# Kernel optimization log

Measured on AMD Instinct MI355X. Metric: run time of the kernel, lower is better.

## Reference

```python
import jax, jax.numpy as jnp
import numpy as np

N = 200000          # nodes
E = 6_400_000       # edges (avg degree 32)
F = 128             # num_node_features
H = 16              # GCN hidden width (hard-coded in module)
MLP_H = 100         # lin1 width (hard-coded)
C = 27              # num_classes (SIDER labels)
G = 4096            # number of graphs in the batch


def setup_inputs() -> dict:
    key = jax.random.key(0)
    ks = jax.random.split(key, 12)
    x = jax.random.normal(ks[0], (N, F), dtype=jnp.float32)
    edge_index = jax.random.randint(ks[1], (2, E), 0, N, dtype=jnp.int64)
    batch_vec = jnp.sort(jax.random.randint(ks[2], (N,), 0, G, dtype=jnp.int64))
    s = 0.05
    W1 = jax.random.normal(ks[3], (F, H), dtype=jnp.float32) * s
    b1 = jnp.zeros((H,), jnp.float32)
    W2 = jax.random.normal(ks[4], (H, H), dtype=jnp.float32) * s
    b2 = jnp.zeros((H,), jnp.float32)
    Wl1 = jax.random.normal(ks[5], (H, MLP_H), dtype=jnp.float32) * s
    bl1 = jnp.zeros((MLP_H,), jnp.float32)
    Wl2 = jax.random.normal(ks[6], (MLP_H, C), dtype=jnp.float32) * s
    bl2 = jnp.zeros((C,), jnp.float32)
    return dict(x=x, edge_index=edge_index, batch_vec=batch_vec,
                W1=W1, b1=b1, W2=W2, b2=b2, Wl1=Wl1, bl1=bl1, Wl2=Wl2, bl2=bl2)


def reference(x, edge_index, batch_vec, W1, b1, W2, b2, Wl1, bl1, Wl2, bl2):
    # PyG GCNConv: add self-loops, symmetric D^-1/2 (A+I) D^-1/2 normalization.
    src, dst = edge_index[0], edge_index[1]
    loop = jnp.arange(N, dtype=edge_index.dtype)
    src_f = jnp.concatenate([src, loop])   # [E+N]
    dst_f = jnp.concatenate([dst, loop])
    deg = jax.ops.segment_sum(jnp.ones(E + N, jnp.float32), dst_f, num_segments=N)
    dinv = jax.lax.rsqrt(deg)              # deg >= 1 due to self-loops
    norm = dinv[src_f] * dinv[dst_f]       # [E+N]

    def gcn_conv(h, W, b):
        h = h @ W                                       # transform first (cheaper: H=16)
        msg = h[src_f] * norm[:, None]                  # gather + scale  [E+N, H]
        return jax.ops.segment_sum(msg, dst_f, num_segments=N) + b

    h = jax.nn.relu(gcn_conv(x, W1, b1))   # dropout: identity in eval mode
    h = gcn_conv(h, W2, b2)
    g = jax.ops.segment_sum(h, batch_vec, num_segments=G)  # global_add_pool [G,H]
    g = jax.nn.relu(g)
    g = jax.nn.relu(g @ Wl1 + bl1)
    return g @ Wl2 + bl2                   # logits [G, C]
```

## Files before the change

### kernel.cpp

```cpp
#include <hip/hip_runtime.h>
#include <hip/hip_bf16.h>

#define NNODES 200000
#define NEDGES 6400000
#define NFEAT  128
#define NH     16
#define NMLP   100
#define NCLS   27
#define NGRAPH 4096

#define BKTSH  10
#define BKTW   1024
#define NBKT   ((NNODES + BKTW - 1) / BKTW)
#define NBLKA  256
#define ABLK   1024
#define EPB    (NEDGES / NBLKA)
#define HSZ    (NBKT * NBLKA)
#define SCANB  1024
#define NSCAN2 ((HSZ + SCANB - 1) / SCANB)
#define CAP    34816

__device__ __forceinline__ unsigned short f2bf(float f) {
    unsigned u = __float_as_uint(f);
    return (unsigned short)((u + 0x7FFF + ((u >> 16) & 1)) >> 16);
}
__device__ __forceinline__ float bf2f(unsigned short s) {
    return __uint_as_float(((unsigned)s) << 16);
}

__global__ __launch_bounds__(ABLK) void k_histA(const int* __restrict__ dst,
                                                int* __restrict__ H) {
    __shared__ int hist[NBKT];
    int tid = threadIdx.x, k = blockIdx.x;
    for (int b = tid; b < NBKT; b += ABLK) hist[b] = 0;
    __syncthreads();
    int base = k * EPB;
    #pragma unroll 4
    for (int i = tid; i < EPB; i += ABLK) {
        int d = __builtin_nontemporal_load(dst + base + i);
        atomicAdd(&hist[d >> BKTSH], 1);
    }
    __syncthreads();
    for (int b = tid; b < NBKT; b += ABLK) H[b * NBLKA + k] = hist[b];
}

__global__ __launch_bounds__(256) void k_scan_part(const int* __restrict__ A,
                                                   int* __restrict__ bsum) {
    __shared__ int sd[256];
    int tid = threadIdx.x;
    int i0 = blockIdx.x * SCANB + tid * 4;
    int s = 0;
    #pragma unroll
    for (int u = 0; u < 4; ++u) {
        int i = i0 + u;
        if (i < HSZ) s += A[i];
    }
    sd[tid] = s;
    __syncthreads();
    for (int off = 128; off > 0; off >>= 1) {
        if (tid < off) sd[tid] += sd[tid + off];
        __syncthreads();
    }
    if (tid == 0) bsum[blockIdx.x] = sd[0];
}

__global__ __launch_bounds__(256) void k_scan_top(int* __restrict__ bsum,
                                                  float* __restrict__ G,
                                                  int* __restrict__ cipad) {
    float4* G4 = (float4*)G;
    int tid = threadIdx.x;
    #pragma unroll
    for (int t = 0; t < (NGRAPH * NH / 4) / 256; ++t)
        G4[tid + t * 256] = make_float4(0.f, 0.f, 0.f, 0.f);
    if (tid < 64) cipad[tid] = 0;

    __shared__ int sd[256];
    int i0 = tid * 4;
    int c[4];
    #pragma unroll
    for (int u = 0; u < 4; ++u) {
        int i = i0 + u;
        c[u] = (i < NSCAN2) ? bsum[i] : 0;
    }
    int mysum = c[0] + c[1] + c[2] + c[3];
    sd[tid] = mysum;
    __syncthreads();
    for (int off = 1; off < 256; off <<= 1) {
        int v = (tid >= off) ? sd[tid - off] : 0;
        __syncthreads();
        sd[tid] += v;
        __syncthreads();
    }
    int base = sd[tid] - mysum;
    #pragma unroll
    for (int u = 0; u < 4; ++u) {
        int i = i0 + u;
        if (i < NSCAN2) { bsum[i] = base; base += c[u]; }
    }
}

__global__ __launch_bounds__(256) void k_scan_final(int* __restrict__ A,
                                                    const int* __restrict__ bsum) {
    __shared__ int sd[256];
    int tid = threadIdx.x;
    int i0 = blockIdx.x * SCANB + tid * 4;
    int c[4];
    #pragma unroll
    for (int u = 0; u < 4; ++u) {
        int i = i0 + u;
        c[u] = (i < HSZ) ? A[i] : 0;
    }
    int mysum = c[0] + c[1] + c[2] + c[3];
    sd[tid] = mysum;
    __syncthreads();
    for (int off = 1; off < 256; off <<= 1) {
        int v = (tid >= off) ? sd[tid - off] : 0;
        __syncthreads();
        sd[tid] += v;
        __syncthreads();
    }
    int base = bsum[blockIdx.x] + sd[tid] - mysum;
    #pragma unroll
    for (int u = 0; u < 4; ++u) {
        int i = i0 + u;
        if (i < HSZ) { A[i] = base; base += c[u]; }
    }
}

__global__ __launch_bounds__(ABLK) void k_scatterA(const int* __restrict__ src,
                                                   const int* __restrict__ dst,
                                                   const int* __restrict__ S,
                                                   int* __restrict__ P) {
    __shared__ int cnt[NBKT];
    int tid = threadIdx.x, k = blockIdx.x;
    for (int b = tid; b < NBKT; b += ABLK) cnt[b] = S[b * NBLKA + k];
    __syncthreads();
    int base = k * EPB;
    #pragma unroll 4
    for (int i = tid; i < EPB; i += ABLK) {
        int d = __builtin_nontemporal_load(dst + base + i);
        int s = __builtin_nontemporal_load(src + base + i);
        int pos = atomicAdd(&cnt[d >> BKTSH], 1);
        P[pos] = ((d & (BKTW - 1)) << 18) | s;
    }
}

__global__ __launch_bounds__(ABLK) void k_csrB(const int* __restrict__ P,
                                               const int* __restrict__ S,
                                               int* __restrict__ rp,
                                               float* __restrict__ dinv,
                                               int* __restrict__ colidx) {
    __shared__ int outl[CAP];
    __shared__ int deg[BKTW];
    __shared__ int wp[BKTW];
    __shared__ int sc[BKTW];
    __shared__ int se[2];
    int b = blockIdx.x, tid = threadIdx.x;
    if (tid == 0) {
        se[0] = S[b * NBLKA];
        se[1] = (b == NBKT - 1) ? NEDGES : S[(b + 1) * NBLKA];
    }
    deg[tid] = 0;
    __syncthreads();
    int start = se[0], end = se[1];

    for (int i = start + tid; i < end; i += ABLK)
        atomicAdd(&deg[P[i] >> 18], 1);
    __syncthreads();

    int myc = deg[tid];
    sc[tid] = myc;
    __syncthreads();
    for (int off = 1; off < BKTW; off <<= 1) {
        int v = (tid >= off) ? sc[tid - off] : 0;
        __syncthreads();
        sc[tid] += v;
        __syncthreads();
    }
    wp[tid] = start + sc[tid] - myc;
    int node = b * BKTW + tid;
    if (node < NNODES) {
        rp[node]   = wp[tid];
        dinv[node] = rsqrtf(1.f + (float)myc);
    }
    if (b == 0 && tid == 0) rp[NNODES] = NEDGES;
    __syncthreads();

    for (int i = start + tid; i < end; i += ABLK) {
        int v = P[i];
        int pos = atomicAdd(&wp[v >> 18], 1);
        int rel = pos - start;
        if (rel < CAP) outl[rel] = v & 0x3FFFF;
        else           colidx[pos] = v & 0x3FFFF;
    }
    __syncthreads();

    int cnt = end - start;
    if (cnt > CAP) cnt = CAP;
    for (int i = tid; i < cnt; i += ABLK)
        colidx[start + i] = outl[i];
}

#define GROWS 64
#define GPAD  129
__global__ __launch_bounds__(256) void k_gemm1(const float* __restrict__ x,
                                               const float* __restrict__ W1,
                                               const float* __restrict__ dinv,
                                               unsigned short* __restrict__ A1b) {
    __shared__ float xt[GROWS * GPAD];
    __shared__ float Ws[NFEAT * NH];
    int tid = threadIdx.x;
    int r0 = blockIdx.x * GROWS;

    #pragma unroll
    for (int t = 0; t < (NFEAT * NH) / 256; ++t)
        Ws[tid + t * 256] = W1[tid + t * 256];

    const float4* xg = (const float4*)(x + (size_t)r0 * NFEAT);
    #pragma unroll
    for (int t = 0; t < (GROWS * NFEAT / 4) / 256; ++t) {
        int fi = tid + t * 256;
        float4 v = xg[fi];
        int row = fi >> 5;
        int c4  = fi & 31;
        float* p = &xt[row * GPAD + c4 * 4];
        p[0] = v.x; p[1] = v.y; p[2] = v.z; p[3] = v.w;
    }
    __syncthreads();

    int r  = tid >> 2;
    int jq = tid & 3;
    float4 acc = make_float4(0.f, 0.f, 0.f, 0.f);
    #pragma unroll 8
    for (int k = 0; k < NFEAT; ++k) {
        float xv = xt[r * GPAD + k];
        float4 w = *(const float4*)&Ws[k * NH + jq * 4];
        acc.x += xv * w.x; acc.y += xv * w.y;
        acc.z += xv * w.z; acc.w += xv * w.w;
    }
    int n = r0 + r;
    float s = dinv[n];
    ushort4 o;
    o.x = f2bf(acc.x * s); o.y = f2bf(acc.y * s);
    o.z = f2bf(acc.z * s); o.w = f2bf(acc.w * s);
    *(ushort4*)&A1b[(size_t)n * NH + jq * 4] = o;
}

__global__ __launch_bounds__(256) void k_gather1(const unsigned short* __restrict__ A1b,
                                                 const int* __restrict__ rp,
                                                 const int* __restrict__ ci,
                                                 const float* __restrict__ dinv,
                                                 const float* __restrict__ b1,
                                                 const float* __restrict__ W2,
                                                 unsigned short* __restrict__ A2b) {
    __shared__ float W2s[NH * NH];
    __shared__ float b1s[NH];
    int tid = threadIdx.x;
    if (tid < NH * NH) W2s[tid] = W2[tid];
    if (tid < NH)      b1s[tid] = b1[tid];
    __syncthreads();

    int nl = tid >> 4, j = tid & 15;
    int n  = blockIdx.x * 16 + nl;
    int r0 = rp[n], r1 = rp[n + 1];

    float acc = bf2f(A1b[(size_t)n * NH + j]);
    for (int k = r0; k < r1; k += 16) {
        int   c[16];
        float v[16];
        #pragma unroll
        for (int u = 0; u < 16; ++u) c[u] = ci[k + u];
        #pragma unroll
        for (int u = 0; u < 16; ++u) v[u] = bf2f(A1b[(size_t)c[u] * NH + j]);
        #pragma unroll
        for (int u = 0; u < 16; ++u) acc += (k + u < r1) ? v[u] : 0.f;
    }

    float h = fmaxf(acc * dinv[n] + b1s[j], 0.f);
    float o = 0.f;
    #pragma unroll
    for (int kk = 0; kk < NH; ++kk)
        o += __shfl(h, kk, 16) * W2s[kk * NH + j];
    A2b[(size_t)n * NH + j] = f2bf(o * dinv[n]);
}

__global__ __launch_bounds__(256) void k_gather2(const unsigned short* __restrict__ A2b,
                                                 const int* __restrict__ rp,
                                                 const int* __restrict__ ci,
                                                 const float* __restrict__ dinv,
                                                 const float* __restrict__ b2,
                                                 const int* __restrict__ batch,
                                                 float* __restrict__ G) {
    __shared__ float b2s[NH];
    int tid = threadIdx.x;
    if (tid < NH) b2s[tid] = b2[tid];
    __syncthreads();

    int nl = tid >> 4, j = tid & 15;
    int n  = blockIdx.x * 16 + nl;
    int r0 = rp[n], r1 = rp[n + 1];

    float acc = bf2f(A2b[(size_t)n * NH + j]);
    for (int k = r0; k < r1; k += 16) {
        int   c[16];
        float v[16];
        #pragma unroll
        for (int u = 0; u < 16; ++u) c[u] = ci[k + u];
        #pragma unroll
        for (int u = 0; u < 16; ++u) v[u] = bf2f(A2b[(size_t)c[u] * NH + j]);
        #pragma unroll
        for (int u = 0; u < 16; ++u) acc += (k + u < r1) ? v[u] : 0.f;
    }

    float h2 = acc * dinv[n] + b2s[j];
    atomicAdd(&G[(size_t)batch[n] * NH + j], h2);
}

__global__ __launch_bounds__(128) void k_head(const float* __restrict__ G,
                                              const float* __restrict__ Wl1,
                                              const float* __restrict__ bl1,
                                              const float* __restrict__ Wl2,
                                              const float* __restrict__ bl2,
                                              float* __restrict__ out) {
    __shared__ float gv[NH];
    __shared__ float g1[NMLP];
    int g = blockIdx.x, tid = threadIdx.x;

    if (tid < NH) gv[tid] = fmaxf(G[(size_t)g * NH + tid], 0.f);
    __syncthreads();

    if (tid < NMLP) {
        float a = bl1[tid];
        #pragma unroll
        for (int k = 0; k < NH; ++k) a += gv[k] * Wl1[k * NMLP + tid];
        g1[tid] = fmaxf(a, 0.f);
    }
    __syncthreads();

    if (tid < NCLS) {
        float a = bl2[tid];
        for (int k = 0; k < NMLP; ++k) a += g1[k] * Wl2[k * NCLS + tid];
        out[(size_t)g * NCLS + tid] = a;
    }
}

extern "C" void kernel_launch(void* const* d_in, const int* in_sizes, int n_in,
                              void* d_out, int out_size, void* d_ws, size_t ws_size,
                              hipStream_t stream) {
    const float* x     = (const float*)d_in[0];
    const int*   edge  = (const int*)d_in[1];
    const int*   batch = (const int*)d_in[2];
    const float* W1    = (const float*)d_in[3];
    const float* b1    = (const float*)d_in[4];
    const float* W2    = (const float*)d_in[5];
    const float* b2    = (const float*)d_in[6];
    const float* Wl1   = (const float*)d_in[7];
    const float* bl1   = (const float*)d_in[8];
    const float* Wl2   = (const float*)d_in[9];
    const float* bl2   = (const float*)d_in[10];
    float*       out   = (float*)d_out;

    char* ws = (char*)d_ws;
    size_t cur = 0;
    auto alloc = [&](size_t bytes) {
        void* p = ws + cur;
        cur += (bytes + 255) & ~(size_t)255;
        return p;
    };
    int*   H      = (int*)  alloc((size_t)HSZ * 4);
    int*   bsum   = (int*)  alloc((size_t)NSCAN2 * 4);
    int*   P      = (int*)  alloc((size_t)NEDGES * 4);
    int*   colidx = (int*)  alloc((size_t)(NEDGES + 64) * 4);
    int*   rp     = (int*)  alloc((size_t)(NNODES + 1) * 4);
    float* dinv   = (float*)alloc((size_t)NNODES * 4);
    float* G      = (float*)alloc((size_t)NGRAPH * NH * 4);
    unsigned short* A1b = (unsigned short*)P;
    unsigned short* A2b = A1b + (size_t)NNODES * NH;

    const int* src = edge;
    const int* dst = edge + NEDGES;

    int nb_gemm = NNODES / GROWS;
    int nb_gath = NNODES / 16;

    k_histA     <<<NBLKA,  ABLK, 0, stream>>>(dst, H);
    k_scan_part <<<NSCAN2, 256, 0, stream>>>(H, bsum);
    k_scan_top  <<<1,      256, 0, stream>>>(bsum, G, colidx + NEDGES);
    k_scan_final<<<NSCAN2, 256, 0, stream>>>(H, bsum);
    k_scatterA  <<<NBLKA,  ABLK, 0, stream>>>(src, dst, H, P);
    k_csrB      <<<NBKT,   ABLK, 0, stream>>>(P, H, rp, dinv, colidx);
    k_gemm1     <<<nb_gemm, 256, 0, stream>>>(x, W1, dinv, A1b);
    k_gather1   <<<nb_gath, 256, 0, stream>>>(A1b, rp, colidx, dinv, b1, W2, A2b);
    k_gather2   <<<nb_gath, 256, 0, stream>>>(A2b, rp, colidx, dinv, b2, batch, G);
    k_head      <<<NGRAPH, 128, 0, stream>>>(G, Wl1, bl1, Wl2, bl2, out);
}
```

Measured before the change: 299.4 us.

## Vectorize edge loads in histogram/scatter, double partition blocks, peel gather tail

The histogram and scatter kernels now read dst/src with 128-bit vector nontemporal loads, four edges per thread iteration, and the number of partition blocks doubles from 256 to 512. The two gather kernels split their neighbor loop into an unmasked full-chunk loop plus one masked tail chunk, which drops the per-element predicate. The larger block count doubles the histogram and scan sizes, and the tail chunk still reads column indices past r1 as before.

```diff
diff --git a/kernel.cpp b/kernel.cpp
--- a/kernel.cpp
+++ b/kernel.cpp
@@ -12,13 +12,16 @@
 #define BKTSH  10
 #define BKTW   1024
 #define NBKT   ((NNODES + BKTW - 1) / BKTW)
-#define NBLKA  256
+#define NBLKA  512
 #define ABLK   1024
 #define EPB    (NEDGES / NBLKA)
+#define EPB4   (EPB / 4)
 #define HSZ    (NBKT * NBLKA)
 #define SCANB  1024
 #define NSCAN2 ((HSZ + SCANB - 1) / SCANB)
 #define CAP    34816
+
+typedef int v4i __attribute__((ext_vector_type(4)));
 
 __device__ __forceinline__ unsigned short f2bf(float f) {
     unsigned u = __float_as_uint(f);
@@ -34,11 +37,14 @@
     int tid = threadIdx.x, k = blockIdx.x;
     for (int b = tid; b < NBKT; b += ABLK) hist[b] = 0;
     __syncthreads();
-    int base = k * EPB;
-    #pragma unroll 4
-    for (int i = tid; i < EPB; i += ABLK) {
-        int d = __builtin_nontemporal_load(dst + base + i);
-        atomicAdd(&hist[d >> BKTSH], 1);
+    const v4i* d4 = (const v4i*)(dst + (size_t)k * EPB);
+    #pragma unroll 2
+    for (int q = tid; q < EPB4; q += ABLK) {
+        v4i d = __builtin_nontemporal_load(d4 + q);
+        atomicAdd(&hist[d.x >> BKTSH], 1);
+        atomicAdd(&hist[d.y >> BKTSH], 1);
+        atomicAdd(&hist[d.z >> BKTSH], 1);
+        atomicAdd(&hist[d.w >> BKTSH], 1);
     }
     __syncthreads();
     for (int b = tid; b < NBKT; b += ABLK) H[b * NBLKA + k] = hist[b];
@@ -135,13 +141,20 @@
     int tid = threadIdx.x, k = blockIdx.x;
     for (int b = tid; b < NBKT; b += ABLK) cnt[b] = S[b * NBLKA + k];
     __syncthreads();
-    int base = k * EPB;
-    #pragma unroll 4
-    for (int i = tid; i < EPB; i += ABLK) {
-        int d = __builtin_nontemporal_load(dst + base + i);
-        int s = __builtin_nontemporal_load(src + base + i);
-        int pos = atomicAdd(&cnt[d >> BKTSH], 1);
-        P[pos] = ((d & (BKTW - 1)) << 18) | s;
+    const v4i* d4 = (const v4i*)(dst + (size_t)k * EPB);
+    const v4i* s4 = (const v4i*)(src + (size_t)k * EPB);
+    #pragma unroll 2
+    for (int q = tid; q < EPB4; q += ABLK) {
+        v4i d = __builtin_nontemporal_load(d4 + q);
+        v4i s = __builtin_nontemporal_load(s4 + q);
+        int p0 = atomicAdd(&cnt[d.x >> BKTSH], 1);
+        int p1 = atomicAdd(&cnt[d.y >> BKTSH], 1);
+        int p2 = atomicAdd(&cnt[d.z >> BKTSH], 1);
+        int p3 = atomicAdd(&cnt[d.w >> BKTSH], 1);
+        P[p0] = ((d.x & (BKTW - 1)) << 18) | s.x;
+        P[p1] = ((d.y & (BKTW - 1)) << 18) | s.y;
+        P[p2] = ((d.z & (BKTW - 1)) << 18) | s.z;
+        P[p3] = ((d.w & (BKTW - 1)) << 18) | s.w;
     }
 }
 
@@ -265,7 +278,18 @@
     int r0 = rp[n], r1 = rp[n + 1];
 
     float acc = bf2f(A1b[(size_t)n * NH + j]);
-    for (int k = r0; k < r1; k += 16) {
+    int k = r0;
+    for (; k + 16 <= r1; k += 16) {
+        int   c[16];
+        float v[16];
+        #pragma unroll
+        for (int u = 0; u < 16; ++u) c[u] = ci[k + u];
+        #pragma unroll
+        for (int u = 0; u < 16; ++u) v[u] = bf2f(A1b[(size_t)c[u] * NH + j]);
+        #pragma unroll
+        for (int u = 0; u < 16; ++u) acc += v[u];
+    }
+    if (k < r1) {
         int   c[16];
         float v[16];
         #pragma unroll
@@ -301,7 +325,18 @@
     int r0 = rp[n], r1 = rp[n + 1];
 
     float acc = bf2f(A2b[(size_t)n * NH + j]);
-    for (int k = r0; k < r1; k += 16) {
+    int k = r0;
+    for (; k + 16 <= r1; k += 16) {
+        int   c[16];
+        float v[16];
+        #pragma unroll
+        for (int u = 0; u < 16; ++u) c[u] = ci[k + u];
+        #pragma unroll
+        for (int u = 0; u < 16; ++u) v[u] = bf2f(A2b[(size_t)c[u] * NH + j]);
+        #pragma unroll
+        for (int u = 0; u < 16; ++u) acc += v[u];
+    }
+    if (k < r1) {
         int   c[16];
         float v[16];
         #pragma unroll
```

New measurement: 290.1 us. 3.1% less time.
